# Performance work log

Measured on AMD Instinct MI355X. Metric: run time of the kernel, lower is better.

## Reference

```python
import jax, jax.numpy as jnp
import numpy as np

C = 16          # cardinality (hard-coded in GraphHead)
E = 1024        # node_encoding_size == representation_size (residual requires equality)
S = 1024        # spatial_head output size (hard-coded Linear(256,1024))
R = 1024        # representation_size
D = R // C      # sub_repr_size = 64
NS, NO = 64, 256
NUM_ITER = 2
EPS = 1e-5


def _w(key, shape, fan_in):
    return jax.random.normal(key, shape, dtype=jnp.float32) * np.float32((2.0 / fan_in) ** 0.5)


def setup_inputs() -> dict:
    key = jax.random.key(0)
    ks = jax.random.split(key, 16)
    inp = {
        'h': jax.random.normal(ks[0], (NS, E), dtype=jnp.float32),
        'o': jax.random.normal(ks[1], (NO, E), dtype=jnp.float32),
        'spatial': jax.random.normal(ks[2], (NS, NO, S), dtype=jnp.float32),
        # attention_head: MultiBranchFusion(2E, 1024, R, 16)
        'att_w1': _w(ks[3], (C, 2 * E, D), 2 * E), 'att_b1': jnp.zeros((C, D), jnp.float32),
        'att_w2': _w(ks[4], (C, S, D), S),         'att_b2': jnp.zeros((C, D), jnp.float32),
        'att_w3': _w(ks[5], (C, D, R), D),         'att_b3': jnp.zeros((C, R), jnp.float32),
        # sub_to_obj: MessageMBF(E, 1024, R, 'subject', 16)
        's2o_w1': _w(ks[6], (C, E, D), E),         's2o_b1': jnp.zeros((C, D), jnp.float32),
        's2o_w2': _w(ks[7], (C, S, D), S),         's2o_b2': jnp.zeros((C, D), jnp.float32),
        's2o_w3': _w(ks[8], (C, D, R), D),         's2o_b3': jnp.zeros((C, R), jnp.float32),
        # obj_to_sub: MessageMBF(E, 1024, R, 'object', 16)
        'o2s_w1': _w(ks[9], (C, E, D), E),         'o2s_b1': jnp.zeros((C, D), jnp.float32),
        'o2s_w2': _w(ks[10], (C, S, D), S),        'o2s_b2': jnp.zeros((C, D), jnp.float32),
        'o2s_w3': _w(ks[11], (C, D, R), D),        'o2s_b3': jnp.zeros((C, R), jnp.float32),
        # adjacency: Linear(R, 1)
        'adj_w': _w(ks[12], (R, 1), R), 'adj_b': jnp.zeros((1,), jnp.float32),
        # LayerNorms
        'ns_g': jnp.ones((E,), jnp.float32), 'ns_b': jnp.zeros((E,), jnp.float32),
        'no_g': jnp.ones((E,), jnp.float32), 'no_b': jnp.zeros((E,), jnp.float32),
    }
    return inp


def _layernorm(x, g, b):
    m = jnp.mean(x, axis=-1, keepdims=True)
    v = jnp.mean((x - m) ** 2, axis=-1, keepdims=True)
    return (x - m) * jax.lax.rsqrt(v + EPS) * g + b


def _mbf_pair(app, spa, w1, b1, w2, b2, w3, b3):
    # app [ns,no,A], spa [ns,no,S] -> [ns,no,R]; sum over C branches of fc3(relu(fc1*fc2))
    a = jnp.einsum('ija,cad->cijd', app, w1) + b1[:, None, None, :]
    s = jnp.einsum('ijs,csd->cijd', spa, w2) + b2[:, None, None, :]
    g = jax.nn.relu(a * s)
    return jnp.einsum('cijd,cdr->ijr', g, w3) + b3.sum(0)


def _msg_subject(h, spa, w1, b1, w2, b2, w3, b3):
    # MessageMBF subject: broadcast fc1(h) [ns,d] against fc2(spa) [ns,no,d]
    a = jnp.einsum('ia,cad->cid', h, w1) + b1[:, None, :]
    s = jnp.einsum('ijs,csd->cijd', spa, w2) + b2[:, None, None, :]
    g = jax.nn.relu(a[:, :, None, :] * s)
    return jnp.einsum('cijd,cdr->ijr', g, w3) + b3.sum(0)  # [ns,no,R]


def _msg_object(o, spa, w1, b1, w2, b2, w3, b3):
    # MessageMBF object: broadcast fc1(o) [no,d] against fc2(spa) [ns,no,d]
    a = jnp.einsum('ja,cad->cjd', o, w1) + b1[:, None, :]
    s = jnp.einsum('ijs,csd->cijd', spa, w2) + b2[:, None, None, :]
    g = jax.nn.relu(a[:, None, :, :] * s)
    return jnp.einsum('cijd,cdr->ijr', g, w3) + b3.sum(0)  # [ns,no,R]


def reference(h, o, spatial,
              att_w1, att_b1, att_w2, att_b2, att_w3, att_b3,
              s2o_w1, s2o_b1, s2o_w2, s2o_b2, s2o_w3, s2o_b3,
              o2s_w1, o2s_b1, o2s_w2, o2s_b2, o2s_w3, o2s_b3,
              adj_w, adj_b, ns_g, ns_b, no_g, no_b):
    ns, no = h.shape[0], o.shape[0]
    for _ in range(NUM_ITER):
        # edge weights via attention MBF on concatenated pair encodings
        pair_app = jnp.concatenate([
            jnp.broadcast_to(h[:, None, :], (ns, no, E)),
            jnp.broadcast_to(o[None, :, :], (ns, no, E)),
        ], axis=-1)
        w = jax.nn.relu(_mbf_pair(pair_app, spatial, att_w1, att_b1, att_w2, att_b2, att_w3, att_b3))
        adj = jnp.einsum('ijr,rk->ij', w, adj_w) + adj_b[0]  # [ns,no]
        # update subject nodes from object messages
        m_o2s = _msg_object(o, spatial, o2s_w1, o2s_b1, o2s_w2, o2s_b2, o2s_w3, o2s_b3)
        msg_h = jax.nn.relu(jnp.einsum('ij,ijr->ir', jax.nn.softmax(adj, axis=1), m_o2s))
        h = _layernorm(h + msg_h, ns_g, ns_b)
        # update object nodes from (updated) subject messages
        m_s2o = _msg_subject(h, spatial, s2o_w1, s2o_b1, s2o_w2, s2o_b2, s2o_w3, s2o_b3)
        msg_o = jax.nn.relu(jnp.einsum('ij,ijr->jr', jax.nn.softmax(adj, axis=0), m_s2o))
        o = _layernorm(o + msg_o, no_g, no_b)
    return jnp.concatenate([h, o], axis=0)  # [ns+no, E]
```

## Files before the change

kernel.cpp:

```cpp
#include <hip/hip_runtime.h>
#include <cstdint>
#include <cstddef>

typedef _Float16 hf;
typedef _Float16 h8v __attribute__((ext_vector_type(8)));
typedef float f4v __attribute__((ext_vector_type(4)));

#define NS 64
#define NO 256
#define MP 16384
#define KD 1024

__device__ __forceinline__ h8v cvt8(float4 a, float4 b) {
    h8v r;
    r[0] = (hf)a.x; r[1] = (hf)a.y; r[2] = (hf)a.z; r[3] = (hf)a.w;
    r[4] = (hf)b.x; r[5] = (hf)b.y; r[6] = (hf)b.z; r[7] = (hf)b.w;
    return r;
}
__device__ __forceinline__ float f4at(const float4& a, const float4& b, int e) {
    const float* p = e < 4 ? (const float*)&a : (const float*)&b;
    return p[e & 3];
}

__global__ void k_pack16(const float* __restrict__ src, hf* __restrict__ dst, int n8) {
    int g = blockIdx.x * 256 + threadIdx.x;
    if (g >= n8) return;
    const float4* s4 = (const float4*)src;
    float4 a = s4[2 * g], b = s4[2 * g + 1];
    *(h8v*)(dst + (size_t)g * 8) = cvt8(a, b);
}

struct RoR { const float* src; hf* dhi; hf* dlo; int Asrc; int aOff; };
struct RoRs { RoR r[7]; };
__global__ void k_reorder16b(RoRs RR) {
    const RoR rt = RR.r[blockIdx.z];
    __shared__ float tile[64][65];
    int c = blockIdx.x, a0 = blockIdx.y * 64;
    int t = threadIdx.x, lx = t & 63, ly = t >> 6;
#pragma unroll
    for (int p = 0; p < 16; ++p) {
        int ar = ly + p * 4;
        tile[ar][lx] = rt.src[(size_t)(c * rt.Asrc + rt.aOff + a0 + ar) * 64 + lx];
    }
    __syncthreads();
#pragma unroll
    for (int p = 0; p < 16; ++p) {
        int d = ly + p * 4;
        float v = tile[lx][d];
        hf h = (hf)v;
        size_t idx = (size_t)(c * 64 + d) * 1024 + a0 + lx;
        rt.dhi[idx] = h;
        if (rt.dlo) rt.dlo[idx] = (hf)(v - (float)h);
    }
}

struct TrR { const float* src; hf* dhi; hf* dlo; };
struct TrRs { TrR r[3]; };
__global__ void k_transpose16b(TrRs RR) {
    const TrR rt = RR.r[blockIdx.z];
    __shared__ float tile[64][65];
    int r0 = blockIdx.x * 64, s0 = blockIdx.y * 64;
    int t = threadIdx.x, lx = t & 63, ly = t >> 6;
#pragma unroll
    for (int p = 0; p < 16; ++p) {
        int srow = ly + p * 4;
        tile[srow][lx] = rt.src[(size_t)(s0 + srow) * 1024 + r0 + lx];
    }
    __syncthreads();
#pragma unroll
    for (int p = 0; p < 16; ++p) {
        int rr = ly + p * 4;
        float v = tile[lx][rr];
        hf h = (hf)v;
        size_t idx = (size_t)(r0 + rr) * 1024 + s0 + lx;
        rt.dhi[idx] = h;
        if (rt.dlo) rt.dlo[idx] = (hf)(v - (float)h);
    }
}

__global__ void k_prep_bc(const float* __restrict__ ab2, const float* __restrict__ ob2,
                          const float* __restrict__ sb2, const float* __restrict__ ab3,
                          const float* __restrict__ ob3, const float* __restrict__ sb3,
                          float* __restrict__ b2cat, float* __restrict__ b3a,
                          float* __restrict__ b3o, float* __restrict__ b3s) {
    int g = blockIdx.x * 256 + threadIdx.x;
    if (g >= 1024) return;
    b2cat[g] = ab2[g]; b2cat[1024 + g] = ob2[g]; b2cat[2048 + g] = sb2[g];
    float sa = 0.f, so = 0.f, ss = 0.f;
    for (int c = 0; c < 16; ++c) {
        sa += ab3[c * 1024 + g];
        so += ob3[c * 1024 + g];
        ss += sb3[c * 1024 + g];
    }
    b3a[g] = sa; b3o[g] = so; b3s[g] = ss;
}

__global__ void k_init_ho(const float* __restrict__ h, const float* __restrict__ o,
                          float* __restrict__ outbuf, hf* __restrict__ h16, hf* __restrict__ o16) {
    int g = blockIdx.x * 256 + threadIdx.x;
    if (g < NS * KD) { float v = h[g]; outbuf[g] = v; h16[g] = (hf)v; }
    int g2 = g - NS * KD;
    if (g2 >= 0 && g2 < NO * KD) { float v = o[g2]; outbuf[NS * KD + g2] = v; o16[g2] = (hf)v; }
}

__global__ __launch_bounds__(256, 2) void k_prep_gemm(
    const hf* __restrict__ sp16,
    const hf* __restrict__ Wah, const hf* __restrict__ Wal,
    const hf* __restrict__ Wo2, const hf* __restrict__ Ws2,
    const float* __restrict__ b2cat,
    hf* __restrict__ Sh, hf* __restrict__ Sl,
    hf* __restrict__ So, hf* __restrict__ Ss) {
    __shared__ hf Ah[4096];
    __shared__ hf Bh[8192];
    __shared__ hf Bl[8192];
    const int tid = threadIdx.x;
    int lin = blockIdx.y * 12 + blockIdx.x;
    int xcd = lin & 7, slot = lin >> 3;
    int xn = slot % 12;
    const int m0 = ((xcd << 4) + slot / 12) * 128;
    const int plane = xn >> 2;
    const int nbase = (xn & 3) * 256;
    const hf* Bb = plane == 0 ? Wah : (plane == 1 ? Wo2 : Ws2);
    const bool hasL = (plane == 0);
    const int lane = tid & 63, wid = tid >> 6;
    const int wm = wid >> 1, wn = wid & 1;
    const int lr = lane & 15, lg = lane >> 4;
    const int srow = tid >> 2, sseg = tid & 3;
    const int wo_ = srow * 32 + (sseg ^ ((srow >> 1) & 3)) * 8;
    const int rsl = (lg ^ ((lr >> 1) & 3)) * 8;

    f4v acc[2][4][4];
    f4v zz; zz[0] = 0.f; zz[1] = 0.f; zz[2] = 0.f; zz[3] = 0.f;
#pragma unroll
    for (int u = 0; u < 2; ++u)
#pragma unroll
        for (int a = 0; a < 4; ++a)
#pragma unroll
            for (int b = 0; b < 4; ++b) acc[u][a][b] = zz;

    const int ko = sseg * 8;
    const hf* pa0 = sp16 + (size_t)(m0 + srow) * KD + ko;
    const hf* pa1 = sp16 + (size_t)(m0 + 64 + srow) * KD + ko;
    const hf* pb00 = Bb + (size_t)(nbase + srow) * KD + ko;
    const hf* pb01 = Bb + (size_t)(nbase + 64 + srow) * KD + ko;
    const hf* pb10 = Bb + (size_t)(nbase + 128 + srow) * KD + ko;
    const hf* pb11 = Bb + (size_t)(nbase + 192 + srow) * KD + ko;
    const hf* ql00 = Wal + (size_t)(nbase + srow) * KD + ko;
    const hf* ql01 = Wal + (size_t)(nbase + 64 + srow) * KD + ko;
    const hf* ql10 = Wal + (size_t)(nbase + 128 + srow) * KD + ko;
    const hf* ql11 = Wal + (size_t)(nbase + 192 + srow) * KD + ko;

    h8v va0, va1, vb00, vb01, vb10, vb11, wb00, wb01, wb10, wb11;
    auto LOAD = [&](int kk) {
        va0 = *(const h8v*)(pa0 + kk); va1 = *(const h8v*)(pa1 + kk);
        vb00 = *(const h8v*)(pb00 + kk); vb01 = *(const h8v*)(pb01 + kk);
        vb10 = *(const h8v*)(pb10 + kk); vb11 = *(const h8v*)(pb11 + kk);
        if (hasL) {
            wb00 = *(const h8v*)(ql00 + kk); wb01 = *(const h8v*)(ql01 + kk);
            wb10 = *(const h8v*)(ql10 + kk); wb11 = *(const h8v*)(ql11 + kk);
        }
    };
    LOAD(0);
    for (int t = 0; t < 32; ++t) {
        __syncthreads();
        *(h8v*)(Ah + wo_) = va0; *(h8v*)(Ah + 2048 + wo_) = va1;
        *(h8v*)(Bh + wo_) = vb00; *(h8v*)(Bh + 2048 + wo_) = vb01;
        *(h8v*)(Bh + 4096 + wo_) = vb10; *(h8v*)(Bh + 6144 + wo_) = vb11;
        if (hasL) {
            *(h8v*)(Bl + wo_) = wb00; *(h8v*)(Bl + 2048 + wo_) = wb01;
            *(h8v*)(Bl + 4096 + wo_) = wb10; *(h8v*)(Bl + 6144 + wo_) = wb11;
        }
        __syncthreads();
        if (t + 1 < 32) LOAD((t + 1) * 32);
        h8v fa[4], fb[4];
#pragma unroll
        for (int x = 0; x < 4; ++x)
            fa[x] = *(const h8v*)(Ah + (wm * 64 + x * 16 + lr) * 32 + rsl);
#pragma unroll
        for (int u = 0; u < 2; ++u) {
#pragma unroll
            for (int x = 0; x < 4; ++x)
                fb[x] = *(const h8v*)(Bh + u * 4096 + (wn * 64 + x * 16 + lr) * 32 + rsl);
#pragma unroll
            for (int mi = 0; mi < 4; ++mi)
#pragma unroll
                for (int ni = 0; ni < 4; ++ni)
                    acc[u][mi][ni] = __builtin_amdgcn_mfma_f32_16x16x32_f16(fa[mi], fb[ni], acc[u][mi][ni], 0, 0, 0);
            if (hasL) {
#pragma unroll
                for (int x = 0; x < 4; ++x)
                    fb[x] = *(const h8v*)(Bl + u * 4096 + (wn * 64 + x * 16 + lr) * 32 + rsl);
#pragma unroll
                for (int mi = 0; mi < 4; ++mi)
#pragma unroll
                    for (int ni = 0; ni < 4; ++ni)
                        acc[u][mi][ni] = __builtin_amdgcn_mfma_f32_16x16x32_f16(fa[mi], fb[ni], acc[u][mi][ni], 0, 0, 0);
            }
        }
    }
#pragma unroll
    for (int u = 0; u < 2; ++u)
#pragma unroll
        for (int mi = 0; mi < 4; ++mi)
#pragma unroll
            for (int ni = 0; ni < 4; ++ni)
#pragma unroll
                for (int r = 0; r < 4; ++r) {
                    int gr = m0 + wm * 64 + mi * 16 + lg * 4 + r;
                    int col = nbase + u * 128 + wn * 64 + ni * 16 + lr;
                    float v = acc[u][mi][ni][r] + b2cat[plane * 1024 + col];
                    size_t idx = (size_t)gr * KD + col;
                    if (plane == 0) {
                        hf hi = (hf)v;
                        Sh[idx] = hi; Sl[idx] = (hf)(v - (float)hi);
                    } else if (plane == 1) So[idx] = (hf)v;
                    else Ss[idx] = (hf)v;
                }
}

__global__ void k_build_g(const hf* __restrict__ Sh, const hf* __restrict__ Sl,
                          const float* __restrict__ e1, const float* __restrict__ e2,
                          hf* __restrict__ Gh) {
    int g = blockIdx.x * 256 + threadIdx.x;
    size_t base = (size_t)g * 8;
    int m = (int)(base >> 10);
    int k = (int)(base & 1023);
    int i = m >> 8, j = m & 255;
    h8v sh = *(const h8v*)(Sh + base);
    h8v sl = *(const h8v*)(Sl + base);
    float4 ex0 = *(const float4*)(e1 + (size_t)i * KD + k);
    float4 ex1 = *(const float4*)(e1 + (size_t)i * KD + k + 4);
    float4 ey0 = *(const float4*)(e2 + (size_t)j * KD + k);
    float4 ey1 = *(const float4*)(e2 + (size_t)j * KD + k + 4);
    h8v gh;
#pragma unroll
    for (int e = 0; e < 8; ++e) {
        float s = (float)sh[e] + (float)sl[e];
        float ee = f4at(ex0, ex1, e) + f4at(ey0, ey1, e);
        float gg = ee * s; gg = gg > 0.f ? gg : 0.f;
        gh[e] = (hf)gg;
    }
    *(h8v*)(Gh + base) = gh;
}

__global__ __launch_bounds__(256, 2) void k_adj_gemm(
    const hf* __restrict__ Gh, const hf* __restrict__ W3h, const hf* __restrict__ W3l,
    const float* __restrict__ b3, const float* __restrict__ aw,
    float* __restrict__ adjv) {
    __shared__ hf Ah[4096];
    __shared__ hf Bh[8192];
    __shared__ hf Bl[8192];
    const int tid = threadIdx.x;
    int lin = blockIdx.y * 4 + blockIdx.x;
    int xcd = lin & 7, slot = lin >> 3;
    const int nbase = (slot & 3) * 256;
    const int m0 = ((xcd << 4) + (slot >> 2)) * 128;
    const int lane = tid & 63, wid = tid >> 6;
    const int wm = wid >> 1, wn = wid & 1;
    const int lr = lane & 15, lg = lane >> 4;
    const int srow = tid >> 2, sseg = tid & 3;
    const int wo_ = srow * 32 + (sseg ^ ((srow >> 1) & 3)) * 8;
    const int rsl = (lg ^ ((lr >> 1) & 3)) * 8;
    const int ar0 = m0 + srow, ar1 = ar0 + 64;
    const int ko = sseg * 8;

    f4v acc[2][4][4];
    f4v zz; zz[0] = 0.f; zz[1] = 0.f; zz[2] = 0.f; zz[3] = 0.f;
#pragma unroll
    for (int u = 0; u < 2; ++u)
#pragma unroll
        for (int a = 0; a < 4; ++a)
#pragma unroll
            for (int b = 0; b < 4; ++b) acc[u][a][b] = zz;

    h8v va0, va1;
    h8v vb00, vb01, vb10, vb11, wb00, wb01, wb10, wb11;
    auto LOAD = [&](int kk) {
        va0 = *(const h8v*)(Gh + (size_t)ar0 * KD + ko + kk);
        va1 = *(const h8v*)(Gh + (size_t)ar1 * KD + ko + kk);
        vb00 = *(const h8v*)(W3h + (size_t)(nbase + srow) * KD + ko + kk);
        vb01 = *(const h8v*)(W3h + (size_t)(nbase + 64 + srow) * KD + ko + kk);
        vb10 = *(const h8v*)(W3h + (size_t)(nbase + 128 + srow) * KD + ko + kk);
        vb11 = *(const h8v*)(W3h + (size_t)(nbase + 192 + srow) * KD + ko + kk);
        wb00 = *(const h8v*)(W3l + (size_t)(nbase + srow) * KD + ko + kk);
        wb01 = *(const h8v*)(W3l + (size_t)(nbase + 64 + srow) * KD + ko + kk);
        wb10 = *(const h8v*)(W3l + (size_t)(nbase + 128 + srow) * KD + ko + kk);
        wb11 = *(const h8v*)(W3l + (size_t)(nbase + 192 + srow) * KD + ko + kk);
    };
    LOAD(0);
    for (int t = 0; t < 32; ++t) {
        __syncthreads();
        *(h8v*)(Ah + wo_) = va0; *(h8v*)(Ah + 2048 + wo_) = va1;
        *(h8v*)(Bh + wo_) = vb00; *(h8v*)(Bh + 2048 + wo_) = vb01;
        *(h8v*)(Bh + 4096 + wo_) = vb10; *(h8v*)(Bh + 6144 + wo_) = vb11;
        *(h8v*)(Bl + wo_) = wb00; *(h8v*)(Bl + 2048 + wo_) = wb01;
        *(h8v*)(Bl + 4096 + wo_) = wb10; *(h8v*)(Bl + 6144 + wo_) = wb11;
        __syncthreads();
        if (t + 1 < 32) LOAD((t + 1) * 32);
        h8v fa[4], fb[4];
#pragma unroll
        for (int x = 0; x < 4; ++x)
            fa[x] = *(const h8v*)(Ah + (wm * 64 + x * 16 + lr) * 32 + rsl);
#pragma unroll
        for (int u = 0; u < 2; ++u) {
#pragma unroll
            for (int x = 0; x < 4; ++x)
                fb[x] = *(const h8v*)(Bh + u * 4096 + (wn * 64 + x * 16 + lr) * 32 + rsl);
#pragma unroll
            for (int mi = 0; mi < 4; ++mi)
#pragma unroll
                for (int ni = 0; ni < 4; ++ni)
                    acc[u][mi][ni] = __builtin_amdgcn_mfma_f32_16x16x32_f16(fa[mi], fb[ni], acc[u][mi][ni], 0, 0, 0);
#pragma unroll
            for (int x = 0; x < 4; ++x)
                fb[x] = *(const h8v*)(Bl + u * 4096 + (wn * 64 + x * 16 + lr) * 32 + rsl);
#pragma unroll
            for (int mi = 0; mi < 4; ++mi)
#pragma unroll
                for (int ni = 0; ni < 4; ++ni)
                    acc[u][mi][ni] = __builtin_amdgcn_mfma_f32_16x16x32_f16(fa[mi], fb[ni], acc[u][mi][ni], 0, 0, 0);
        }
    }
    float b3v[2][4], awv[2][4];
#pragma unroll
    for (int u = 0; u < 2; ++u)
#pragma unroll
        for (int ni = 0; ni < 4; ++ni) {
            int gc = nbase + u * 128 + wn * 64 + ni * 16 + lr;
            b3v[u][ni] = b3[gc]; awv[u][ni] = aw[gc];
        }
#pragma unroll
    for (int mi = 0; mi < 4; ++mi)
#pragma unroll
        for (int r = 0; r < 4; ++r) {
            float part = 0.f;
#pragma unroll
            for (int u = 0; u < 2; ++u)
#pragma unroll
                for (int ni = 0; ni < 4; ++ni) {
                    float w = acc[u][mi][ni][r] + b3v[u][ni];
                    w = w > 0.f ? w : 0.f;
                    part += w * awv[u][ni];
                }
            part += __shfl_xor(part, 1);
            part += __shfl_xor(part, 2);
            part += __shfl_xor(part, 4);
            part += __shfl_xor(part, 8);
            if (lr == 0) atomicAdd(adjv + m0 + wm * 64 + mi * 16 + lg * 4 + r, part);
        }
}

struct SRoute { const hf* A; const hf* Bh; const hf* Bl; float* C; const float* bias; int m0; int M; };
struct SRoutes { SRoute r[5]; };

__global__ __launch_bounds__(256) void k_small(SRoutes RR) {
    const SRoute rt = RR.r[blockIdx.y];
    __shared__ hf Ah[4096];
    __shared__ hf Bh[4096];
    __shared__ hf Bl[4096];
    const int tid = threadIdx.x;
    const int n0 = blockIdx.x * 128;
    const int kbeg = blockIdx.z * 128;
    const int lane = tid & 63, wid = tid >> 6;
    const int wm = wid >> 1, wn = wid & 1;
    const int lr = lane & 15, lg = lane >> 4;
    const int srow = tid >> 2, sseg = tid & 3;
    const int wo_ = srow * 32 + (sseg ^ ((srow >> 1) & 3)) * 8;
    const int rsl = (lg ^ ((lr >> 1) & 3)) * 8;
    int ar0 = rt.m0 + srow;      if (ar0 >= rt.M) ar0 = rt.M - 1;
    int ar1 = rt.m0 + 64 + srow; if (ar1 >= rt.M) ar1 = rt.M - 1;
    const bool hasL = rt.Bl != nullptr;
    const int ko = kbeg + sseg * 8;

    f4v acc[4][4];
    f4v zz; zz[0] = 0.f; zz[1] = 0.f; zz[2] = 0.f; zz[3] = 0.f;
#pragma unroll
    for (int a = 0; a < 4; ++a)
#pragma unroll
        for (int b = 0; b < 4; ++b) acc[a][b] = zz;

    h8v va0, va1, vb0, vb1, wb0, wb1;
    auto LOAD = [&](int kk) {
        va0 = *(const h8v*)(rt.A + (size_t)ar0 * KD + ko + kk);
        va1 = *(const h8v*)(rt.A + (size_t)ar1 * KD + ko + kk);
        vb0 = *(const h8v*)(rt.Bh + (size_t)(n0 + srow) * KD + ko + kk);
        vb1 = *(const h8v*)(rt.Bh + (size_t)(n0 + 64 + srow) * KD + ko + kk);
        if (hasL) {
            wb0 = *(const h8v*)(rt.Bl + (size_t)(n0 + srow) * KD + ko + kk);
            wb1 = *(const h8v*)(rt.Bl + (size_t)(n0 + 64 + srow) * KD + ko + kk);
        }
    };
    LOAD(0);
    for (int t = 0; t < 4; ++t) {
        __syncthreads();
        *(h8v*)(Ah + wo_) = va0; *(h8v*)(Ah + 2048 + wo_) = va1;
        *(h8v*)(Bh + wo_) = vb0; *(h8v*)(Bh + 2048 + wo_) = vb1;
        if (hasL) { *(h8v*)(Bl + wo_) = wb0; *(h8v*)(Bl + 2048 + wo_) = wb1; }
        __syncthreads();
        if (t + 1 < 4) LOAD((t + 1) * 32);
        h8v fa[4], fb[4];
#pragma unroll
        for (int x = 0; x < 4; ++x) {
            fa[x] = *(const h8v*)(Ah + (wm * 64 + x * 16 + lr) * 32 + rsl);
            fb[x] = *(const h8v*)(Bh + (wn * 64 + x * 16 + lr) * 32 + rsl);
        }
#pragma unroll
        for (int mi = 0; mi < 4; ++mi)
#pragma unroll
            for (int ni = 0; ni < 4; ++ni)
                acc[mi][ni] = __builtin_amdgcn_mfma_f32_16x16x32_f16(fa[mi], fb[ni], acc[mi][ni], 0, 0, 0);
        if (hasL) {
#pragma unroll
            for (int x = 0; x < 4; ++x)
                fb[x] = *(const h8v*)(Bl + (wn * 64 + x * 16 + lr) * 32 + rsl);
#pragma unroll
            for (int mi = 0; mi < 4; ++mi)
#pragma unroll
                for (int ni = 0; ni < 4; ++ni)
                    acc[mi][ni] = __builtin_amdgcn_mfma_f32_16x16x32_f16(fa[mi], fb[ni], acc[mi][ni], 0, 0, 0);
        }
    }
#pragma unroll
    for (int mi = 0; mi < 4; ++mi)
#pragma unroll
        for (int ni = 0; ni < 4; ++ni)
#pragma unroll
            for (int r = 0; r < 4; ++r) {
                int gr = rt.m0 + wm * 64 + mi * 16 + lg * 4 + r;
                int gc = n0 + wn * 64 + ni * 16 + lr;
                if (gr < rt.M) {
                    float v = acc[mi][ni][r];
                    if (rt.bias && blockIdx.z == 0) v += rt.bias[gc];
                    atomicAdd(rt.C + (size_t)gr * KD + gc, v);
                }
            }
}

__global__ void k_softmax_rows(const float* __restrict__ adj, float* __restrict__ p) {
    __shared__ float red[256];
    int i = blockIdx.x, j = threadIdx.x;
    float x = adj[i * 256 + j];
    red[j] = x; __syncthreads();
    for (int s = 128; s > 0; s >>= 1) { if (j < s) red[j] = fmaxf(red[j], red[j + s]); __syncthreads(); }
    float mx = red[0]; __syncthreads();
    float e = __expf(x - mx);
    red[j] = e; __syncthreads();
    for (int s = 128; s > 0; s >>= 1) { if (j < s) red[j] += red[j + s]; __syncthreads(); }
    p[i * 256 + j] = e / red[0];
}

__global__ void k_softmax_cols(const float* __restrict__ adj, float* __restrict__ q) {
    int j = blockIdx.x, i = threadIdx.x;
    float x = adj[i * 256 + j];
    float mx = x;
#pragma unroll
    for (int off = 32; off > 0; off >>= 1) mx = fmaxf(mx, __shfl_xor(mx, off));
    float e = __expf(x - mx);
    float s = e;
#pragma unroll
    for (int off = 32; off > 0; off >>= 1) s += __shfl_xor(s, off);
    q[i * 256 + j] = e / s;
}

__global__ void k_build_Gh(const hf* __restrict__ S, const float* __restrict__ aF,
                           const float* __restrict__ p, hf* __restrict__ Gh) {
    __shared__ float pl[256];
    int i = blockIdx.x;
    int k = blockIdx.y * 256 + threadIdx.x;
    pl[threadIdx.x] = p[i * 256 + threadIdx.x];
    __syncthreads();
    const hf* sp = S + (size_t)(i * 256) * KD + k;
    float acc = 0.f;
#pragma unroll 4
    for (int j = 0; j < 256; ++j) {
        float a = aF[(size_t)j * KD + k];
        float s = (float)sp[(size_t)j * KD];
        float g = a * s; g = g > 0.f ? g : 0.f;
        acc += pl[j] * g;
    }
    Gh[(size_t)i * KD + k] = (hf)acc;
}

__global__ void k_build_Go(const hf* __restrict__ S, const float* __restrict__ aF,
                           const float* __restrict__ q, hf* __restrict__ Go) {
    __shared__ float ql[64];
    int j = blockIdx.x;
    int k = blockIdx.y * 256 + threadIdx.x;
    if (threadIdx.x < 64) ql[threadIdx.x] = q[threadIdx.x * 256 + j];
    __syncthreads();
    const hf* sp = S + (size_t)j * KD + k;
    float acc = 0.f;
#pragma unroll 4
    for (int i = 0; i < 64; ++i) {
        float a = aF[(size_t)i * KD + k];
        float s = (float)sp[(size_t)(i * 256) * KD];
        float g = a * s; g = g > 0.f ? g : 0.f;
        acc += ql[i] * g;
    }
    Go[(size_t)j * KD + k] = (hf)acc;
}

__global__ void k_ln_update(float* __restrict__ x, const float* __restrict__ msg,
                            const float* __restrict__ b3, const float* __restrict__ gamma,
                            const float* __restrict__ beta, hf* __restrict__ x16) {
    __shared__ float red[256];
    int r = blockIdx.x, t = threadIdx.x;
    float v[4];
    float s = 0.f;
#pragma unroll
    for (int e = 0; e < 4; ++e) {
        int idx = t + e * 256;
        float mm = msg[(size_t)r * KD + idx] + b3[idx];
        mm = mm > 0.f ? mm : 0.f;
        v[e] = x[(size_t)r * KD + idx] + mm;
        s += v[e];
    }
    red[t] = s; __syncthreads();
    for (int st = 128; st > 0; st >>= 1) { if (t < st) red[t] += red[t + st]; __syncthreads(); }
    float mean = red[0] * (1.f / 1024.f);
    __syncthreads();
    float s2 = 0.f;
#pragma unroll
    for (int e = 0; e < 4; ++e) { float d = v[e] - mean; s2 += d * d; }
    red[t] = s2; __syncthreads();
    for (int st = 128; st > 0; st >>= 1) { if (t < st) red[t] += red[t + st]; __syncthreads(); }
    float var = red[0] * (1.f / 1024.f);
    float rstd = rsqrtf(var + 1e-5f);
#pragma unroll
    for (int e = 0; e < 4; ++e) {
        int idx = t + e * 256;
        float y = (v[e] - mean) * rstd * gamma[idx] + beta[idx];
        x[(size_t)r * KD + idx] = y;
        x16[(size_t)r * KD + idx] = (hf)y;
    }
}

extern "C" void kernel_launch(void* const* d_in, const int* in_sizes, int n_in,
                              void* d_out, int out_size, void* d_ws, size_t ws_size,
                              hipStream_t stream) {
    const float* h_in    = (const float*)d_in[0];
    const float* o_in    = (const float*)d_in[1];
    const float* spatial = (const float*)d_in[2];
    const float* att_w1  = (const float*)d_in[3];
    const float* att_b1  = (const float*)d_in[4];
    const float* att_w2  = (const float*)d_in[5];
    const float* att_b2  = (const float*)d_in[6];
    const float* att_w3  = (const float*)d_in[7];
    const float* att_b3  = (const float*)d_in[8];
    const float* s2o_w1  = (const float*)d_in[9];
    const float* s2o_b1  = (const float*)d_in[10];
    const float* s2o_w2  = (const float*)d_in[11];
    const float* s2o_b2  = (const float*)d_in[12];
    const float* s2o_w3  = (const float*)d_in[13];
    const float* s2o_b3  = (const float*)d_in[14];
    const float* o2s_w1  = (const float*)d_in[15];
    const float* o2s_b1  = (const float*)d_in[16];
    const float* o2s_w2  = (const float*)d_in[17];
    const float* o2s_b2  = (const float*)d_in[18];
    const float* o2s_w3  = (const float*)d_in[19];
    const float* o2s_b3  = (const float*)d_in[20];
    const float* adj_w   = (const float*)d_in[21];
    const float* ns_g    = (const float*)d_in[23];
    const float* ns_b    = (const float*)d_in[24];
    const float* no_g    = (const float*)d_in[25];
    const float* no_b    = (const float*)d_in[26];

    char* ws = (char*)d_ws;
    size_t off = 0;
    auto alloc = [&](size_t bytes) -> char* {
        char* pp = ws + off;
        off += (bytes + 255) & ~(size_t)255;
        return pp;
    };
    const size_t PLANE = (size_t)MP * KD * sizeof(hf);
    const size_t WMAT  = (size_t)1024 * 1024 * sizeof(hf);
    hf* S_att_h = (hf*)alloc(PLANE);
    hf* S_att_l = (hf*)alloc(PLANE);
    hf* S_o2s   = (hf*)alloc(PLANE);
    hf* S_s2o   = (hf*)alloc(PLANE);
    hf* gA_h    = (hf*)alloc(PLANE);
    hf* sp16    = gA_h;
    hf* W2att_h = (hf*)alloc(WMAT); hf* W2att_l = (hf*)alloc(WMAT);
    hf* W2o2s   = (hf*)alloc(WMAT);
    hf* W2s2o   = (hf*)alloc(WMAT);
    hf* W1ah_h  = (hf*)alloc(WMAT); hf* W1ah_l  = (hf*)alloc(WMAT);
    hf* W1ao_h  = (hf*)alloc(WMAT); hf* W1ao_l  = (hf*)alloc(WMAT);
    hf* W1o2s   = (hf*)alloc(WMAT);
    hf* W1s2o   = (hf*)alloc(WMAT);
    hf* W3a_h   = (hf*)alloc(WMAT); hf* W3a_l   = (hf*)alloc(WMAT);
    hf* W3o     = (hf*)alloc(WMAT);
    hf* W3s     = (hf*)alloc(WMAT);
    float* b2cat = (float*)alloc(3072 * 4);
    float* b3a   = (float*)alloc(1024 * 4);
    float* b3o   = (float*)alloc(1024 * 4);
    float* b3s   = (float*)alloc(1024 * 4);
    float* fc1h = (float*)alloc((size_t)NS * KD * 4);
    float* fc1o = (float*)alloc((size_t)NO * KD * 4);
    float* aO2S = (float*)alloc((size_t)NO * KD * 4);
    float* aS2O = (float*)alloc((size_t)NS * KD * 4);
    float* msgh = (float*)alloc((size_t)NS * KD * 4);
    float* msgo = (float*)alloc((size_t)NO * KD * 4);
    float* adjv = (float*)alloc((size_t)MP * 4);
    char* zend_ = (char*)(adjv + MP);
    size_t zlen = (size_t)(zend_ - (char*)fc1h);
    float* pbuf = (float*)alloc((size_t)MP * 4);
    float* qbuf = (float*)alloc((size_t)MP * 4);
    hf* h16 = (hf*)alloc((size_t)NS * KD * sizeof(hf));
    hf* o16 = (hf*)alloc((size_t)NO * KD * sizeof(hf));
    hf* Gh  = (hf*)alloc((size_t)NS * KD * sizeof(hf));
    hf* Go  = (hf*)alloc((size_t)NO * KD * sizeof(hf));

    float* hbuf = (float*)d_out;
    float* obuf = (float*)d_out + NS * KD;

    k_pack16<<<dim3(MP * KD / 8 / 256), 256, 0, stream>>>(spatial, sp16, MP * KD / 8);
    {
        RoRs R;
        R.r[0] = { att_w2, W2att_h, W2att_l, 1024, 0 };
        R.r[1] = { o2s_w2, W2o2s, nullptr, 1024, 0 };
        R.r[2] = { s2o_w2, W2s2o, nullptr, 1024, 0 };
        R.r[3] = { att_w1, W1ah_h, W1ah_l, 2048, 0 };
        R.r[4] = { att_w1, W1ao_h, W1ao_l, 2048, 1024 };
        R.r[5] = { o2s_w1, W1o2s, nullptr, 1024, 0 };
        R.r[6] = { s2o_w1, W1s2o, nullptr, 1024, 0 };
        k_reorder16b<<<dim3(16, 16, 7), 256, 0, stream>>>(R);
    }
    {
        TrRs T;
        T.r[0] = { att_w3, W3a_h, W3a_l };
        T.r[1] = { o2s_w3, W3o, nullptr };
        T.r[2] = { s2o_w3, W3s, nullptr };
        k_transpose16b<<<dim3(16, 16, 3), 256, 0, stream>>>(T);
    }
    k_prep_bc<<<dim3(4), 256, 0, stream>>>(att_b2, o2s_b2, s2o_b2, att_b3, o2s_b3, s2o_b3,
                                           b2cat, b3a, b3o, b3s);
    k_init_ho<<<dim3(1280), 256, 0, stream>>>(h_in, o_in, (float*)d_out, h16, o16);
    k_prep_gemm<<<dim3(12, 128), 256, 0, stream>>>(sp16, W2att_h, W2att_l, W2o2s, W2s2o,
                                                   b2cat, S_att_h, S_att_l, S_o2s, S_s2o);

    for (int it = 0; it < 2; ++it) {
        hipMemsetAsync(fc1h, 0, zlen, stream);
        {
            SRoutes R;
            R.r[0] = { h16, W1ah_h, W1ah_l, fc1h, att_b1, 0,   NS };
            R.r[1] = { o16, W1ao_h, W1ao_l, fc1o, nullptr, 0,   NO };
            R.r[2] = { o16, W1ao_h, W1ao_l, fc1o, nullptr, 128, NO };
            R.r[3] = { o16, W1o2s,  nullptr, aO2S, o2s_b1, 0,   NO };
            R.r[4] = { o16, W1o2s,  nullptr, aO2S, o2s_b1, 128, NO };
            k_small<<<dim3(8, 5, 8), 256, 0, stream>>>(R);
        }
        k_build_g<<<dim3(MP * KD / 8 / 256), 256, 0, stream>>>(S_att_h, S_att_l, fc1h, fc1o, gA_h);
        k_adj_gemm<<<dim3(4, 128), 256, 0, stream>>>(gA_h, W3a_h, W3a_l, b3a, adj_w, adjv);
        k_softmax_rows<<<dim3(NS), 256, 0, stream>>>(adjv, pbuf);
        k_softmax_cols<<<dim3(NO), 64, 0, stream>>>(adjv, qbuf);
        k_build_Gh<<<dim3(NS, 4), 256, 0, stream>>>(S_o2s, aO2S, pbuf, Gh);
        {
            SRoutes R;
            R.r[0] = { Gh, W3o, nullptr, msgh, nullptr, 0, NS };
            k_small<<<dim3(8, 1, 8), 256, 0, stream>>>(R);
        }
        k_ln_update<<<dim3(NS), 256, 0, stream>>>(hbuf, msgh, b3o, ns_g, ns_b, h16);
        {
            SRoutes R;
            R.r[0] = { h16, W1s2o, nullptr, aS2O, s2o_b1, 0, NS };
            k_small<<<dim3(8, 1, 8), 256, 0, stream>>>(R);
        }
        k_build_Go<<<dim3(NO, 4), 256, 0, stream>>>(S_s2o, aS2O, qbuf, Go);
        {
            SRoutes R;
            R.r[0] = { Go, W3s, nullptr, msgo, nullptr, 0,   NO };
            R.r[1] = { Go, W3s, nullptr, msgo, nullptr, 128, NO };
            k_small<<<dim3(8, 2, 8), 256, 0, stream>>>(R);
        }
        k_ln_update<<<dim3(NO), 256, 0, stream>>>(obuf, msgo, b3s, no_g, no_b, o16);
    }
    (void)in_sizes; (void)n_in; (void)out_size; (void)ws_size;
}
```

Baseline: 629.4 us.

## Shrink adj GEMM N-tile to 128 for more blocks, merge softmax kernels

The adjacency GEMM tile goes from 128x256 to 128x128, doubling the grid to 1024 blocks. This halves accumulator registers and LDS per block so occupancy can rise (launch bounds raised to 3). The cost is that each A tile is loaded from global memory twice as often, and there are twice as many atomic adds into adjv. The row and column softmax kernels are also merged into one launch, with four columns per 256-thread block, to save a launch.

Result: slower. 647.9 us (+2.9%).

```diff
diff --git a/kernel.cpp b/kernel.cpp
--- a/kernel.cpp
+++ b/kernel.cpp
@@ -243,18 +243,18 @@
     *(h8v*)(Gh + base) = gh;
 }
 
-__global__ __launch_bounds__(256, 2) void k_adj_gemm(
+__global__ __launch_bounds__(256, 3) void k_adj_gemm(
     const hf* __restrict__ Gh, const hf* __restrict__ W3h, const hf* __restrict__ W3l,
     const float* __restrict__ b3, const float* __restrict__ aw,
     float* __restrict__ adjv) {
     __shared__ hf Ah[4096];
-    __shared__ hf Bh[8192];
-    __shared__ hf Bl[8192];
+    __shared__ hf Bh[4096];
+    __shared__ hf Bl[4096];
     const int tid = threadIdx.x;
-    int lin = blockIdx.y * 4 + blockIdx.x;
+    int lin = blockIdx.y * 8 + blockIdx.x;
     int xcd = lin & 7, slot = lin >> 3;
-    const int nbase = (slot & 3) * 256;
-    const int m0 = ((xcd << 4) + (slot >> 2)) * 128;
+    const int nbase = (slot & 7) * 128;
+    const int m0 = ((xcd << 4) + (slot >> 3)) * 128;
     const int lane = tid & 63, wid = tid >> 6;
     const int wm = wid >> 1, wn = wid & 1;
     const int lr = lane & 15, lg = lane >> 4;
@@ -264,84 +264,67 @@
     const int ar0 = m0 + srow, ar1 = ar0 + 64;
     const int ko = sseg * 8;
 
-    f4v acc[2][4][4];
+    f4v acc[4][4];
     f4v zz; zz[0] = 0.f; zz[1] = 0.f; zz[2] = 0.f; zz[3] = 0.f;
 #pragma unroll
-    for (int u = 0; u < 2; ++u)
-#pragma unroll
-        for (int a = 0; a < 4; ++a)
-#pragma unroll
-            for (int b = 0; b < 4; ++b) acc[u][a][b] = zz;
-
-    h8v va0, va1;
-    h8v vb00, vb01, vb10, vb11, wb00, wb01, wb10, wb11;
+    for (int a = 0; a < 4; ++a)
+#pragma unroll
+        for (int b = 0; b < 4; ++b) acc[a][b] = zz;
+
+    h8v va0, va1, vb0, vb1, wb0, wb1;
     auto LOAD = [&](int kk) {
         va0 = *(const h8v*)(Gh + (size_t)ar0 * KD + ko + kk);
         va1 = *(const h8v*)(Gh + (size_t)ar1 * KD + ko + kk);
-        vb00 = *(const h8v*)(W3h + (size_t)(nbase + srow) * KD + ko + kk);
-        vb01 = *(const h8v*)(W3h + (size_t)(nbase + 64 + srow) * KD + ko + kk);
-        vb10 = *(const h8v*)(W3h + (size_t)(nbase + 128 + srow) * KD + ko + kk);
-        vb11 = *(const h8v*)(W3h + (size_t)(nbase + 192 + srow) * KD + ko + kk);
-        wb00 = *(const h8v*)(W3l + (size_t)(nbase + srow) * KD + ko + kk);
-        wb01 = *(const h8v*)(W3l + (size_t)(nbase + 64 + srow) * KD + ko + kk);
-        wb10 = *(const h8v*)(W3l + (size_t)(nbase + 128 + srow) * KD + ko + kk);
-        wb11 = *(const h8v*)(W3l + (size_t)(nbase + 192 + srow) * KD + ko + kk);
+        vb0 = *(const h8v*)(W3h + (size_t)(nbase + srow) * KD + ko + kk);
+        vb1 = *(const h8v*)(W3h + (size_t)(nbase + 64 + srow) * KD + ko + kk);
+        wb0 = *(const h8v*)(W3l + (size_t)(nbase + srow) * KD + ko + kk);
+        wb1 = *(const h8v*)(W3l + (size_t)(nbase + 64 + srow) * KD + ko + kk);
     };
     LOAD(0);
     for (int t = 0; t < 32; ++t) {
         __syncthreads();
         *(h8v*)(Ah + wo_) = va0; *(h8v*)(Ah + 2048 + wo_) = va1;
-        *(h8v*)(Bh + wo_) = vb00; *(h8v*)(Bh + 2048 + wo_) = vb01;
-        *(h8v*)(Bh + 4096 + wo_) = vb10; *(h8v*)(Bh + 6144 + wo_) = vb11;
-        *(h8v*)(Bl + wo_) = wb00; *(h8v*)(Bl + 2048 + wo_) = wb01;
-        *(h8v*)(Bl + 4096 + wo_) = wb10; *(h8v*)(Bl + 6144 + wo_) = wb11;
+        *(h8v*)(Bh + wo_) = vb0; *(h8v*)(Bh + 2048 + wo_) = vb1;
+        *(h8v*)(Bl + wo_) = wb0; *(h8v*)(Bl + 2048 + wo_) = wb1;
         __syncthreads();
         if (t + 1 < 32) LOAD((t + 1) * 32);
         h8v fa[4], fb[4];
 #pragma unroll
+        for (int x = 0; x < 4; ++x) {
+            fa[x] = *(const h8v*)(Ah + (wm * 64 + x * 16 + lr) * 32 + rsl);
+            fb[x] = *(const h8v*)(Bh + (wn * 64 + x * 16 + lr) * 32 + rsl);
+        }
+#pragma unroll
+        for (int mi = 0; mi < 4; ++mi)
+#pragma unroll
+            for (int ni = 0; ni < 4; ++ni)
+                acc[mi][ni] = __builtin_amdgcn_mfma_f32_16x16x32_f16(fa[mi], fb[ni], acc[mi][ni], 0, 0, 0);
+#pragma unroll
         for (int x = 0; x < 4; ++x)
-            fa[x] = *(const h8v*)(Ah + (wm * 64 + x * 16 + lr) * 32 + rsl);
-#pragma unroll
-        for (int u = 0; u < 2; ++u) {
-#pragma unroll
-            for (int x = 0; x < 4; ++x)
-                fb[x] = *(const h8v*)(Bh + u * 4096 + (wn * 64 + x * 16 + lr) * 32 + rsl);
-#pragma unroll
-            for (int mi = 0; mi < 4; ++mi)
-#pragma unroll
-                for (int ni = 0; ni < 4; ++ni)
-                    acc[u][mi][ni] = __builtin_amdgcn_mfma_f32_16x16x32_f16(fa[mi], fb[ni], acc[u][mi][ni], 0, 0, 0);
-#pragma unroll
-            for (int x = 0; x < 4; ++x)
-                fb[x] = *(const h8v*)(Bl + u * 4096 + (wn * 64 + x * 16 + lr) * 32 + rsl);
-#pragma unroll
-            for (int mi = 0; mi < 4; ++mi)
-#pragma unroll
-                for (int ni = 0; ni < 4; ++ni)
-                    acc[u][mi][ni] = __builtin_amdgcn_mfma_f32_16x16x32_f16(fa[mi], fb[ni], acc[u][mi][ni], 0, 0, 0);
-        }
-    }
-    float b3v[2][4], awv[2][4];
-#pragma unroll
-    for (int u = 0; u < 2; ++u)
-#pragma unroll
-        for (int ni = 0; ni < 4; ++ni) {
-            int gc = nbase + u * 128 + wn * 64 + ni * 16 + lr;
-            b3v[u][ni] = b3[gc]; awv[u][ni] = aw[gc];
-        }
+            fb[x] = *(const h8v*)(Bl + (wn * 64 + x * 16 + lr) * 32 + rsl);
+#pragma unroll
+        for (int mi = 0; mi < 4; ++mi)
+#pragma unroll
+            for (int ni = 0; ni < 4; ++ni)
+                acc[mi][ni] = __builtin_amdgcn_mfma_f32_16x16x32_f16(fa[mi], fb[ni], acc[mi][ni], 0, 0, 0);
+    }
+    float b3v[4], awv[4];
+#pragma unroll
+    for (int ni = 0; ni < 4; ++ni) {
+        int gc = nbase + wn * 64 + ni * 16 + lr;
+        b3v[ni] = b3[gc]; awv[ni] = aw[gc];
+    }
 #pragma unroll
     for (int mi = 0; mi < 4; ++mi)
 #pragma unroll
         for (int r = 0; r < 4; ++r) {
             float part = 0.f;
 #pragma unroll
-            for (int u = 0; u < 2; ++u)
-#pragma unroll
-                for (int ni = 0; ni < 4; ++ni) {
-                    float w = acc[u][mi][ni][r] + b3v[u][ni];
-                    w = w > 0.f ? w : 0.f;
-                    part += w * awv[u][ni];
-                }
+            for (int ni = 0; ni < 4; ++ni) {
+                float w = acc[mi][ni][r] + b3v[ni];
+                w = w > 0.f ? w : 0.f;
+                part += w * awv[ni];
+            }
             part += __shfl_xor(part, 1);
             part += __shfl_xor(part, 2);
             part += __shfl_xor(part, 4);
@@ -436,30 +419,33 @@
             }
 }
 
-__global__ void k_softmax_rows(const float* __restrict__ adj, float* __restrict__ p) {
-    __shared__ float red[256];
-    int i = blockIdx.x, j = threadIdx.x;
-    float x = adj[i * 256 + j];
-    red[j] = x; __syncthreads();
-    for (int s = 128; s > 0; s >>= 1) { if (j < s) red[j] = fmaxf(red[j], red[j + s]); __syncthreads(); }
-    float mx = red[0]; __syncthreads();
-    float e = __expf(x - mx);
-    red[j] = e; __syncthreads();
-    for (int s = 128; s > 0; s >>= 1) { if (j < s) red[j] += red[j + s]; __syncthreads(); }
-    p[i * 256 + j] = e / red[0];
-}
-
-__global__ void k_softmax_cols(const float* __restrict__ adj, float* __restrict__ q) {
-    int j = blockIdx.x, i = threadIdx.x;
-    float x = adj[i * 256 + j];
-    float mx = x;
-#pragma unroll
-    for (int off = 32; off > 0; off >>= 1) mx = fmaxf(mx, __shfl_xor(mx, off));
-    float e = __expf(x - mx);
-    float s = e;
-#pragma unroll
-    for (int off = 32; off > 0; off >>= 1) s += __shfl_xor(s, off);
-    q[i * 256 + j] = e / s;
+__global__ void k_softmax_both(const float* __restrict__ adj, float* __restrict__ p,
+                               float* __restrict__ q) {
+    int b = blockIdx.x;
+    if (b < NS) {
+        __shared__ float red[256];
+        int i = b, j = threadIdx.x;
+        float x = adj[i * 256 + j];
+        red[j] = x; __syncthreads();
+        for (int s = 128; s > 0; s >>= 1) { if (j < s) red[j] = fmaxf(red[j], red[j + s]); __syncthreads(); }
+        float mx = red[0]; __syncthreads();
+        float e = __expf(x - mx);
+        red[j] = e; __syncthreads();
+        for (int s = 128; s > 0; s >>= 1) { if (j < s) red[j] += red[j + s]; __syncthreads(); }
+        p[i * 256 + j] = e / red[0];
+    } else {
+        int j = (b - NS) * 4 + (threadIdx.x >> 6);
+        int i = threadIdx.x & 63;
+        float x = adj[i * 256 + j];
+        float mx = x;
+#pragma unroll
+        for (int off = 32; off > 0; off >>= 1) mx = fmaxf(mx, __shfl_xor(mx, off));
+        float e = __expf(x - mx);
+        float s = e;
+#pragma unroll
+        for (int off = 32; off > 0; off >>= 1) s += __shfl_xor(s, off);
+        q[i * 256 + j] = e / s;
+    }
 }
 
 __global__ void k_build_Gh(const hf* __restrict__ S, const float* __restrict__ aF,
@@ -650,9 +636,8 @@
             k_small<<<dim3(8, 5, 8), 256, 0, stream>>>(R);
         }
         k_build_g<<<dim3(MP * KD / 8 / 256), 256, 0, stream>>>(S_att_h, S_att_l, fc1h, fc1o, gA_h);
-        k_adj_gemm<<<dim3(4, 128), 256, 0, stream>>>(gA_h, W3a_h, W3a_l, b3a, adj_w, adjv);
-        k_softmax_rows<<<dim3(NS), 256, 0, stream>>>(adjv, pbuf);
-        k_softmax_cols<<<dim3(NO), 64, 0, stream>>>(adjv, qbuf);
+        k_adj_gemm<<<dim3(8, 128), 256, 0, stream>>>(gA_h, W3a_h, W3a_l, b3a, adj_w, adjv);
+        k_softmax_both<<<dim3(NS + NO / 4), 256, 0, stream>>>(adjv, pbuf, qbuf);
         k_build_Gh<<<dim3(NS, 4), 256, 0, stream>>>(S_o2s, aO2S, pbuf, Gh);
         {
             SRoutes R;
```
